# Kernel optimization log

Hardware: AMD Instinct MI355X
Metric: run time of the kernel (lower is better)

## Reference

```python
import jax, jax.numpy as jnp
import numpy as np

T, B, E, H = 2048, 2, 1024, 16
Dh = E // H


def setup_inputs() -> dict:
    key = jax.random.key(0)
    ks = jax.random.split(key, 5)
    s = 0.02
    query = jax.random.normal(ks[0], (T, B, E), dtype=jnp.float32)
    Wq = jax.random.normal(ks[1], (E, E), dtype=jnp.float32) * s
    Wk = jax.random.normal(ks[2], (E, E), dtype=jnp.float32) * s
    Wv = jax.random.normal(ks[3], (E, E), dtype=jnp.float32) * s
    Wo = jax.random.normal(ks[4], (E, E), dtype=jnp.float32) * s
    bq = jnp.zeros((E,), jnp.float32)
    bk = jnp.zeros((E,), jnp.float32)
    bv = jnp.zeros((E,), jnp.float32)
    bo = jnp.zeros((E,), jnp.float32)
    # additive causal mask: 0 on/below diagonal, -inf above (standard fairseq usage)
    neg = jnp.finfo(jnp.float32).min
    attn_mask = jnp.where(jnp.triu(jnp.ones((T, T), jnp.bool_), k=1), neg, 0.0).astype(jnp.float32)
    return {"query": query, "Wq": Wq, "bq": bq, "Wk": Wk, "bk": bk,
            "Wv": Wv, "bv": bv, "Wo": Wo, "bo": bo, "attn_mask": attn_mask}


def reference(query, Wq, bq, Wk, bk, Wv, bv, Wo, bo, attn_mask):
    t, b, e = query.shape
    scale = Dh ** -0.5
    # self-attention projections (nn.Linear: x @ W.T + b)
    q = (query @ Wq.T + bq) * scale  # [T,B,E]
    k = query @ Wk.T + bk
    v = query @ Wv.T + bv
    # [T, B*H, Dh] -> [B*H, T, Dh]
    q = q.reshape(t, b * H, Dh).transpose(1, 0, 2)
    k = k.reshape(t, b * H, Dh).transpose(1, 0, 2)
    v = v.reshape(t, b * H, Dh).transpose(1, 0, 2)
    # explicit bmm -> softmax -> bmm (materializes [B*H, T, T])
    attn_weights = jnp.einsum('btd,bsd->bts', q, k) + attn_mask[None, :, :]
    attn_probs = jax.nn.softmax(attn_weights, axis=-1)
    attn = jnp.einsum('bts,bsd->btd', attn_probs, v)  # [B*H, T, Dh]
    attn = attn.transpose(1, 0, 2).reshape(t, b, e)  # [T,B,E]
    out = attn @ Wo.T + bo
    return out
```

## Files before the change

### kernel.cpp

```cpp
#include <hip/hip_runtime.h>


typedef __attribute__((ext_vector_type(8))) short   s16x8;
typedef __attribute__((ext_vector_type(4))) float   f32x4;
typedef __attribute__((ext_vector_type(2))) __fp16  f16x2;
typedef __attribute__((ext_vector_type(4))) __fp16  f16x4;

#define MFMA16(a, b, c) __builtin_amdgcn_mfma_f32_16x16x32_bf16((a), (b), (c), 0, 0, 0)
#define MFMApv(a, b, c) __builtin_amdgcn_mfma_f32_16x16x16f16((a), (b), (c), 0, 0, 0)

static __device__ __forceinline__ unsigned short f2bf(float f) {
    unsigned u = __float_as_uint(f);
    unsigned r = u + 0x7fffu + ((u >> 16) & 1u);
    return (unsigned short)(r >> 16);
}

static __device__ __forceinline__ void gl2lds16(const void* g, void* l) {
    __builtin_amdgcn_global_load_lds(
        (const __attribute__((address_space(1))) unsigned int*)g,
        (__attribute__((address_space(3))) unsigned int*)l, 16, 0, 0);
}

__global__ __launch_bounds__(256) void cvt_all(const float* __restrict__ query,
                                               const float* __restrict__ w0,
                                               const float* __restrict__ w1,
                                               const float* __restrict__ w2,
                                               const float* __restrict__ w3,
                                               unsigned short* __restrict__ Xb,
                                               unsigned short* __restrict__ Wcat) {
    const int bx = blockIdx.x;
    if (bx < 4096) {
        const int i = threadIdx.x;
        const float4 f = reinterpret_cast<const float4*>(query + (size_t)bx * 1024)[i];
        ushort4 u;
        u.x = f2bf(f.x); u.y = f2bf(f.y); u.z = f2bf(f.z); u.w = f2bf(f.w);
        const int mrow = (bx & 1) * 2048 + (bx >> 1);
        reinterpret_cast<ushort4*>(Xb + (size_t)mrow * 1024)[i] = u;
    } else {
        const int j   = bx - 4096;
        const int sel = j >> 10;
        const int i   = (j & 1023) * 256 + threadIdx.x;
        const float* src = (sel == 0) ? w0 : (sel == 1) ? w1 : (sel == 2) ? w2 : w3;
        const float4 f = reinterpret_cast<const float4*>(src)[i];
        ushort4 u;
        u.x = f2bf(f.x); u.y = f2bf(f.y); u.z = f2bf(f.z); u.w = f2bf(f.w);
        reinterpret_cast<ushort4*>(Wcat + (size_t)sel * 1048576)[i] = u;
    }
}

__global__ __launch_bounds__(512, 2) void gemm_qkv(const unsigned short* __restrict__ A,
                                                   const unsigned short* __restrict__ W,
                                                   const float* __restrict__ b0,
                                                   const float* __restrict__ b1,
                                                   const float* __restrict__ b2,
                                                   unsigned short* __restrict__ outQK,
                                                   __fp16* __restrict__ outV) {
    __shared__ __align__(16) unsigned short smem[65536];

    const int tid  = threadIdx.x;
    const int w    = tid >> 6;
    const int lane = tid & 63;
    const int quad = lane >> 4;
    const int c    = lane & 15;
    const int wm   = w >> 2;
    const int wn   = w & 3;

    const int id   = blockIdx.x;
    const int xcd  = id & 7;
    const int slot = id >> 3;
    const int m0 = (xcd * 2 + (slot & 1)) * 256;
    const int n0 = (slot >> 1) * 256;

    f32x4 acc[8][4];
    #pragma unroll
    for (int mi = 0; mi < 8; ++mi)
        #pragma unroll
        for (int ni = 0; ni < 4; ++ni) acc[mi][ni] = (f32x4){0.f, 0.f, 0.f, 0.f};

    const int srow = tid >> 3;
    const int g    = (tid & 7) ^ (srow & 7);
    const unsigned short* aG = A + (size_t)(m0 + srow) * 1024 + g * 8;
    const unsigned short* wG = W + (size_t)(n0 + srow) * 1024 + g * 8;
    const int loff = tid * 8;

#define STA(buf, u, k0) gl2lds16(aG + (k0) + (u) * 65536, &smem[(buf) * 32768 + (u) * 4096 + loff])
#define STB(buf, u, k0) gl2lds16(wG + (k0) + (u) * 65536, &smem[(buf) * 32768 + 16384 + (u) * 4096 + loff])

    STB(0, 0, 0); STB(0, 1, 0); STB(0, 2, 0); STB(0, 3, 0);
    STA(0, 0, 0); STA(0, 2, 0); STA(0, 1, 0); STA(0, 3, 0);
    asm volatile("s_waitcnt vmcnt(2)" ::: "memory");
    asm volatile("s_barrier" ::: "memory");

    const int cs  = c & 7;
    const int ch0 = (quad ^ cs) << 3;
    const int ch1 = ((4 + quad) ^ cs) << 3;

    s16x8 af[4][2], bf[4][2];

    #pragma unroll
    for (int mi = 0; mi < 4; ++mi) {
        const int row = (wm * 128 + mi * 16 + c) * 64;
        af[mi][0] = *reinterpret_cast<const s16x8*>(&smem[row + ch0]);
        af[mi][1] = *reinterpret_cast<const s16x8*>(&smem[row + ch1]);
    }
    #pragma unroll
    for (int ni = 0; ni < 4; ++ni) {
        const int row = (wn * 64 + ni * 16 + c) * 64;
        bf[ni][0] = *reinterpret_cast<const s16x8*>(&smem[16384 + row + ch0]);
        bf[ni][1] = *reinterpret_cast<const s16x8*>(&smem[16384 + row + ch1]);
    }

    #pragma unroll 1
    for (int t = 0; t < 16; ++t) {
        const unsigned short* Al = &smem[(t & 1) * 32768];
        const int  nb   = (t & 1) ^ 1;
        const int  kn   = (t + 1) * 64;
        const bool more = (t < 15);

        if (more) {
            STB(nb, 0, kn); STB(nb, 1, kn); STB(nb, 2, kn); STB(nb, 3, kn);
            STA(nb, 0, kn); STA(nb, 2, kn); STA(nb, 1, kn); STA(nb, 3, kn);
        }

        __builtin_amdgcn_s_setprio(1);
        #pragma unroll
        for (int mi = 0; mi < 4; ++mi)
            #pragma unroll
            for (int ni = 0; ni < 4; ++ni) {
                acc[mi][ni] = MFMA16(af[mi][0], bf[ni][0], acc[mi][ni]);
                acc[mi][ni] = MFMA16(af[mi][1], bf[ni][1], acc[mi][ni]);
            }
        __builtin_amdgcn_s_setprio(0);

        if (more) asm volatile("s_waitcnt vmcnt(8)" ::: "memory");
        else      asm volatile("s_waitcnt vmcnt(0)" ::: "memory");
        asm volatile("s_barrier" ::: "memory");

        #pragma unroll
        for (int mi = 0; mi < 4; ++mi) {
            const int row = (wm * 128 + 64 + mi * 16 + c) * 64;
            af[mi][0] = *reinterpret_cast<const s16x8*>(&Al[row + ch0]);
            af[mi][1] = *reinterpret_cast<const s16x8*>(&Al[row + ch1]);
        }
        __builtin_amdgcn_s_setprio(1);
        #pragma unroll
        for (int mi = 0; mi < 4; ++mi)
            #pragma unroll
            for (int ni = 0; ni < 4; ++ni) {
                acc[4 + mi][ni] = MFMA16(af[mi][0], bf[ni][0], acc[4 + mi][ni]);
                acc[4 + mi][ni] = MFMA16(af[mi][1], bf[ni][1], acc[4 + mi][ni]);
            }
        __builtin_amdgcn_s_setprio(0);

        if (more) {
            asm volatile("s_waitcnt vmcnt(2)" ::: "memory");
            asm volatile("s_barrier" ::: "memory");
            const unsigned short* An = &smem[nb * 32768];
            #pragma unroll
            for (int mi = 0; mi < 4; ++mi) {
                const int row = (wm * 128 + mi * 16 + c) * 64;
                af[mi][0] = *reinterpret_cast<const s16x8*>(&An[row + ch0]);
                af[mi][1] = *reinterpret_cast<const s16x8*>(&An[row + ch1]);
            }
            #pragma unroll
            for (int ni = 0; ni < 4; ++ni) {
                const int row = (wn * 64 + ni * 16 + c) * 64;
                bf[ni][0] = *reinterpret_cast<const s16x8*>(&An[16384 + row + ch0]);
                bf[ni][1] = *reinterpret_cast<const s16x8*>(&An[16384 + row + ch1]);
            }
        }
    }
#undef STA
#undef STB

    if (n0 < 2048) {
        const float scale = (n0 < 1024) ? 0.18033688011112042f : 1.0f;
        const float* bias = (n0 < 1024) ? b0 : b1;
        #pragma unroll
        for (int ni = 0; ni < 4; ++ni) {
            const int n = n0 + wn * 64 + ni * 16 + c;
            const float bval = bias[n & 1023];
            #pragma unroll
            for (int mi = 0; mi < 8; ++mi)
                #pragma unroll
                for (int r = 0; r < 4; ++r) {
                    const int m = m0 + wm * 128 + mi * 16 + quad * 4 + r;
                    outQK[(size_t)m * 2048 + n] = f2bf((acc[mi][ni][r] + bval) * scale);
                }
        }
    } else {
        __fp16* lds16 = reinterpret_cast<__fp16*>(smem);
        #pragma unroll 1
        for (int tn = 0; tn < 2; ++tn) {
            __syncthreads();
            if ((wn >> 1) == tn) {
                #pragma unroll
                for (int ni = 0; ni < 4; ++ni) {
                    const int nLoc = (wn & 1) * 64 + ni * 16 + c;
                    const float bval = b2[(n0 - 2048) + tn * 128 + nLoc];
                    #pragma unroll
                    for (int mi = 0; mi < 8; ++mi) {
                        const int mLoc = mi * 16 + quad * 4;
                        const f16x2 lo = __builtin_amdgcn_cvt_pkrtz(acc[mi][ni][0] + bval,
                                                                    acc[mi][ni][1] + bval);
                        const f16x2 hi = __builtin_amdgcn_cvt_pkrtz(acc[mi][ni][2] + bval,
                                                                    acc[mi][ni][3] + bval);
                        uint2 st;
                        st.x = __builtin_bit_cast(unsigned int, lo);
                        st.y = __builtin_bit_cast(unsigned int, hi);
                        const int phys = wm * 16384 + nLoc * 128 +
                                         (((mLoc >> 3) ^ (nLoc & 15)) << 3) + (mLoc & 7);
                        *reinterpret_cast<uint2*>(&lds16[phys]) = st;
                    }
                }
            }
            __syncthreads();
            const int np   = tid >> 1;
            const int rg   = np >> 7;
            const int nLoc = np & 127;
            const int vcol = (n0 - 2048) + tn * 128 + nLoc;
            const int bb = m0 >> 11;
            const int tbase = (m0 & 2047) + rg * 128;
            __fp16* vdst = outV + ((size_t)((bb * 16 + (vcol >> 6)) * 64 + (vcol & 63))) * 2048 + tbase;
            #pragma unroll
            for (int j = 0; j < 8; ++j) {
                const int lc = (tid & 1) * 8 + j;
                *reinterpret_cast<uint4*>(vdst + lc * 8) =
                    *reinterpret_cast<const uint4*>(
                        &lds16[rg * 16384 + nLoc * 128 + ((lc ^ (nLoc & 15)) << 3)]);
            }
        }
    }
}

__global__ __launch_bounds__(256) void gemm_out(const unsigned short* __restrict__ A,
                                                const unsigned short* __restrict__ W,
                                                const float* __restrict__ bias,
                                                float* __restrict__ outF) {
    __shared__ __align__(16) unsigned short Al[2][64 * 64];
    __shared__ __align__(16) unsigned short Bl[2][128 * 64];

    const int tid  = threadIdx.x;
    const int w    = tid >> 6;
    const int lane = tid & 63;
    const int quad = lane >> 4;
    const int c    = lane & 15;

    const int id   = blockIdx.x;
    const int xcd  = id & 7;
    const int slot = id >> 3;
    const int m0 = (xcd * 8 + (slot & 7)) * 64;
    const int n0 = (slot >> 3) * 128;

    f32x4 acc[8];
    #pragma unroll
    for (int ni = 0; ni < 8; ++ni) acc[ni] = (f32x4){0.f, 0.f, 0.f, 0.f};

    const int srow = tid >> 3;
    const int g    = (tid & 7) ^ (srow & 7);
    const unsigned short* aG = A + (size_t)(m0 + srow) * 1024 + g * 8;
    const unsigned short* wG = W + (size_t)(n0 + srow) * 1024 + g * 8;
    const int loff = tid * 8;

    const int cs = (c & 7);

    gl2lds16(aG,             &Al[0][loff]);
    gl2lds16(aG + 32 * 1024, &Al[0][loff + 2048]);
    #pragma unroll
    for (int i = 0; i < 4; ++i)
        gl2lds16(wG + i * 32 * 1024, &Bl[0][loff + i * 2048]);

    #pragma unroll 1
    for (int kk = 0; kk < 16; ++kk) {
        __syncthreads();
        if (kk < 15) {
            const int k0n = (kk + 1) * 64;
            const int nb  = (kk + 1) & 1;
            gl2lds16(aG + k0n,             &Al[nb][loff]);
            gl2lds16(aG + k0n + 32 * 1024, &Al[nb][loff + 2048]);
            #pragma unroll
            for (int i = 0; i < 4; ++i)
                gl2lds16(wG + k0n + i * 32 * 1024, &Bl[nb][loff + i * 2048]);
        }
        const int cb = kk & 1;
        const int arow = (w * 16 + c) * 64;
        const s16x8 af0 = *reinterpret_cast<const s16x8*>(&Al[cb][arow + ((quad ^ cs) << 3)]);
        const s16x8 af1 = *reinterpret_cast<const s16x8*>(&Al[cb][arow + (((4 + quad) ^ cs) << 3)]);
        __builtin_amdgcn_s_setprio(1);
        #pragma unroll
        for (int ni = 0; ni < 8; ++ni) {
            const int brow = (ni * 16 + c) * 64;
            const s16x8 bf0 = *reinterpret_cast<const s16x8*>(&Bl[cb][brow + ((quad ^ cs) << 3)]);
            const s16x8 bf1 = *reinterpret_cast<const s16x8*>(&Bl[cb][brow + (((4 + quad) ^ cs) << 3)]);
            acc[ni] = MFMA16(af0, bf0, acc[ni]);
            acc[ni] = MFMA16(af1, bf1, acc[ni]);
        }
        __builtin_amdgcn_s_setprio(0);
    }

    #pragma unroll
    for (int ni = 0; ni < 8; ++ni) {
        const int n = n0 + ni * 16 + c;
        const float bval = bias[n];
        const int m = m0 + w * 16 + quad * 4;
        const int bb = m >> 11, t = m & 2047;
        #pragma unroll
        for (int r = 0; r < 4; ++r)
            outF[(size_t)(2 * (t + r) + bb) * 1024 + n] = acc[ni][r] + bval;
    }
}

__global__ __launch_bounds__(256, 4) void attn_kernel(const unsigned short* __restrict__ QKb,
                                                      const __fp16* __restrict__ Vt,
                                                      unsigned short* __restrict__ Ob) {
    __shared__ unsigned short Kl[2][2][64][32];
    __shared__ __fp16 Vl[2][64][64];

    const int tid  = threadIdx.x;
    const int w    = tid >> 6;
    const int lane = tid & 63;
    const int quad = lane >> 4;
    const int c    = lane & 15;

    const int id = blockIdx.x;
    const int bh = (id & 7) * 4 + ((id >> 3) & 3);
    const int kidx = id >> 5;
    const int rr   = kidx >> 3, jj = kidx & 7;
    const int a    = (rr & 1) ? (24 - 8 * rr + jj) : (31 - 8 * rr - jj);
    const int bB = bh >> 4, h = bh & 15;
    const int t0 = a * 64;
    const int trg = t0 + w * 16;
    const int nIt = a + 1;

    const unsigned short* qp = QKb + (size_t)(bB * 2048 + trg + c) * 2048 + h * 64 + quad * 8;
    const s16x8 aq0 = *reinterpret_cast<const s16x8*>(qp);
    const s16x8 aq1 = *reinterpret_cast<const s16x8*>(qp + 32);

    const int lr4 = lane >> 2, sl4 = lane & 3;
    const unsigned short* kSrc = QKb + (size_t)(bB * 2048 + w * 16 + lr4) * 2048
                                 + 1024 + h * 64 + (sl4 ^ ((lane >> 3) & 3)) * 8;
    const int vr8 = lane >> 3, sl8 = lane & 7;
    const __fp16* vSrcA = Vt + (size_t)(bh * 64 + w * 16 + vr8) * 2048 + (sl8 ^ vr8) * 8;
    const __fp16* vSrcB = vSrcA + (size_t)8 * 2048;

    f32x4 acc[4];
    float l = 0.f;
    #pragma unroll
    for (int dt = 0; dt < 4; ++dt) acc[dt] = (f32x4){0.f, 0.f, 0.f, 0.f};

    const int kswz = (quad ^ ((c >> 1) & 3)) * 8;

    {
        gl2lds16(kSrc,      &Kl[0][0][w * 16 + lr4][sl4 * 8]);
        gl2lds16(kSrc + 32, &Kl[0][1][w * 16 + lr4][sl4 * 8]);
        gl2lds16(vSrcA,     &Vl[0][w * 16 + vr8][sl8 * 8]);
        gl2lds16(vSrcB,     &Vl[0][w * 16 + 8 + vr8][sl8 * 8]);
    }

    for (int it = 0; it < nIt; ++it) {
        const int buf = it & 1;
        __syncthreads();
        if (it + 1 < nIt) {
            const size_t s1 = (size_t)(it + 1) * 64;
            const int nb = buf ^ 1;
            gl2lds16(kSrc + s1 * 2048,      &Kl[nb][0][w * 16 + lr4][sl4 * 8]);
            gl2lds16(kSrc + s1 * 2048 + 32, &Kl[nb][1][w * 16 + lr4][sl4 * 8]);
            gl2lds16(vSrcA + s1,            &Vl[nb][w * 16 + vr8][sl8 * 8]);
            gl2lds16(vSrcB + s1,            &Vl[nb][w * 16 + 8 + vr8][sl8 * 8]);
        }

        s16x8 kf[4][2];
        #pragma unroll
        for (int ns = 0; ns < 4; ++ns) {
            kf[ns][0] = *reinterpret_cast<const s16x8*>(&Kl[buf][0][ns * 16 + c][kswz]);
            kf[ns][1] = *reinterpret_cast<const s16x8*>(&Kl[buf][1][ns * 16 + c][kswz]);
        }
        f16x4 vf[4][4];
        #pragma unroll
        for (int dt = 0; dt < 4; ++dt)
            #pragma unroll
            for (int ch = 0; ch < 4; ++ch) {
                const int phys = ((2 * ch + (quad >> 1)) ^ (c & 7)) * 8 + (quad & 1) * 4;
                vf[dt][ch] = *reinterpret_cast<const f16x4*>(&Vl[buf][dt * 16 + c][phys]);
            }

        const int s0 = it * 64;
        const bool diag = (it == a);
        f32x4 sT[4];
        __builtin_amdgcn_s_setprio(1);
        #pragma unroll
        for (int ns = 0; ns < 4; ++ns) {
            f32x4 z = (f32x4){0.f, 0.f, 0.f, 0.f};
            z = MFMA16(kf[ns][0], aq0, z);
            sT[ns] = MFMA16(kf[ns][1], aq1, z);
        }
        __builtin_amdgcn_s_setprio(0);
        f16x4 pf[4];
        float lp = 0.f;
        #pragma unroll
        for (int ns = 0; ns < 4; ++ns) {
            float pv[4];
            #pragma unroll
            for (int r = 0; r < 4; ++r) pv[r] = __builtin_amdgcn_exp2f(sT[ns][r]);
            if (diag) {
                const int sb = s0 + ns * 16 + quad * 4;
                const int qg = trg + c;
                #pragma unroll
                for (int r = 0; r < 4; ++r) if (sb + r > qg) pv[r] = 0.f;
            }
            lp += (pv[0] + pv[1]) + (pv[2] + pv[3]);
            const f16x2 lo = __builtin_amdgcn_cvt_pkrtz(pv[0], pv[1]);
            const f16x2 hi = __builtin_amdgcn_cvt_pkrtz(pv[2], pv[3]);
            pf[ns] = __builtin_shufflevector(lo, hi, 0, 1, 2, 3);
        }
        l += lp;
        __builtin_amdgcn_s_setprio(1);
        #pragma unroll
        for (int dt = 0; dt < 4; ++dt)
            #pragma unroll
            for (int ns = 0; ns < 4; ++ns)
                acc[dt] = MFMApv(vf[dt][ns], pf[ns], acc[dt]);
        __builtin_amdgcn_s_setprio(0);
    }

    float lv = l;
    lv += __shfl_xor(lv, 16);
    lv += __shfl_xor(lv, 32);
    const float inv = 1.0f / lv;
    const size_t base = (size_t)(bB * 2048 + trg + c) * 1024 + h * 64;
    #pragma unroll
    for (int dt = 0; dt < 4; ++dt) {
        const unsigned u0 = (unsigned)f2bf(acc[dt][0] * inv)
                          | ((unsigned)f2bf(acc[dt][1] * inv) << 16);
        const unsigned u1 = (unsigned)f2bf(acc[dt][2] * inv)
                          | ((unsigned)f2bf(acc[dt][3] * inv) << 16);
        uint2 st; st.x = u0; st.y = u1;
        *reinterpret_cast<uint2*>(Ob + base + dt * 16 + quad * 4) = st;
    }
}

extern "C" void kernel_launch(void* const* d_in, const int* in_sizes, int n_in,
                              void* d_out, int out_size, void* d_ws, size_t ws_size,
                              hipStream_t stream) {
    const float* query = (const float*)d_in[0];
    const float* Wq    = (const float*)d_in[1];
    const float* bq    = (const float*)d_in[2];
    const float* Wk    = (const float*)d_in[3];
    const float* bk    = (const float*)d_in[4];
    const float* Wv    = (const float*)d_in[5];
    const float* bv    = (const float*)d_in[6];
    const float* Wo    = (const float*)d_in[7];
    const float* bo    = (const float*)d_in[8];

    float* out = (float*)d_out;

    unsigned short* ws    = (unsigned short*)d_ws;
    unsigned short* Xbf   = ws;
    unsigned short* Wcat  = Xbf  + (size_t)4096 * 1024;
    unsigned short* QKb   = Wcat + (size_t)4 * 1024 * 1024;
    __fp16*         Vtw   = (__fp16*)(QKb + (size_t)4096 * 2048);
    unsigned short* attnb = (unsigned short*)(Vtw + (size_t)32 * 64 * 2048);

    cvt_all<<<8192, 256, 0, stream>>>(query, Wq, Wk, Wv, Wo, Xbf, Wcat);

    gemm_qkv<<<192, 512, 0, stream>>>(Xbf, Wcat, bq, bk, bv, QKb, Vtw);

    attn_kernel<<<1024, 256, 0, stream>>>(QKb, Vtw, attnb);

    gemm_out<<<512, 256, 0, stream>>>(attnb, Wcat + (size_t)3 * 1024 * 1024,
                                      bo, out);
}
```

Baseline: 193.5 us.

## Shrink QKV GEMM N-tile to 192 so grid fills all 256 CUs

The QKV projection GEMM's output tile width drops from 256 to 192 columns. The grid grows from 192 to 256 blocks, matching the CU count on MI355X and removing idle CUs. The epilogue is reworked so a tile can straddle the K/V boundary (column 2048): QK columns take the bf16 path, V columns go through a reworked LDS transpose into the fp16 transposed V buffer. The smaller tile lowers arithmetic intensity per block and adds branchy epilogue logic.

```diff
diff --git a/kernel.cpp b/kernel.cpp
--- a/kernel.cpp
+++ b/kernel.cpp
@@ -55,7 +55,7 @@
                                                    const float* __restrict__ b2,
                                                    unsigned short* __restrict__ outQK,
                                                    __fp16* __restrict__ outV) {
-    __shared__ __align__(16) unsigned short smem[65536];
+    __shared__ __align__(16) unsigned short smem[57344];
 
     const int tid  = threadIdx.x;
     const int w    = tid >> 6;
@@ -69,13 +69,13 @@
     const int xcd  = id & 7;
     const int slot = id >> 3;
     const int m0 = (xcd * 2 + (slot & 1)) * 256;
-    const int n0 = (slot >> 1) * 256;
-
-    f32x4 acc[8][4];
+    const int n0 = (slot >> 1) * 192;
+
+    f32x4 acc[8][3];
     #pragma unroll
     for (int mi = 0; mi < 8; ++mi)
         #pragma unroll
-        for (int ni = 0; ni < 4; ++ni) acc[mi][ni] = (f32x4){0.f, 0.f, 0.f, 0.f};
+        for (int ni = 0; ni < 3; ++ni) acc[mi][ni] = (f32x4){0.f, 0.f, 0.f, 0.f};
 
     const int srow = tid >> 3;
     const int g    = (tid & 7) ^ (srow & 7);
@@ -83,10 +83,10 @@
     const unsigned short* wG = W + (size_t)(n0 + srow) * 1024 + g * 8;
     const int loff = tid * 8;
 
-#define STA(buf, u, k0) gl2lds16(aG + (k0) + (u) * 65536, &smem[(buf) * 32768 + (u) * 4096 + loff])
-#define STB(buf, u, k0) gl2lds16(wG + (k0) + (u) * 65536, &smem[(buf) * 32768 + 16384 + (u) * 4096 + loff])
-
-    STB(0, 0, 0); STB(0, 1, 0); STB(0, 2, 0); STB(0, 3, 0);
+#define STA(buf, u, k0) gl2lds16(aG + (k0) + (u) * 65536, &smem[(buf) * 28672 + (u) * 4096 + loff])
+#define STB(buf, u, k0) gl2lds16(wG + (k0) + (u) * 65536, &smem[(buf) * 28672 + 16384 + (u) * 4096 + loff])
+
+    STB(0, 0, 0); STB(0, 1, 0); STB(0, 2, 0);
     STA(0, 0, 0); STA(0, 2, 0); STA(0, 1, 0); STA(0, 3, 0);
     asm volatile("s_waitcnt vmcnt(2)" ::: "memory");
     asm volatile("s_barrier" ::: "memory");
@@ -95,7 +95,7 @@
     const int ch0 = (quad ^ cs) << 3;
     const int ch1 = ((4 + quad) ^ cs) << 3;
 
-    s16x8 af[4][2], bf[4][2];
+    s16x8 af[4][2], bf[3][2];
 
     #pragma unroll
     for (int mi = 0; mi < 4; ++mi) {
@@ -104,21 +104,21 @@
         af[mi][1] = *reinterpret_cast<const s16x8*>(&smem[row + ch1]);
     }
     #pragma unroll
-    for (int ni = 0; ni < 4; ++ni) {
-        const int row = (wn * 64 + ni * 16 + c) * 64;
+    for (int ni = 0; ni < 3; ++ni) {
+        const int row = (wn * 48 + ni * 16 + c) * 64;
         bf[ni][0] = *reinterpret_cast<const s16x8*>(&smem[16384 + row + ch0]);
         bf[ni][1] = *reinterpret_cast<const s16x8*>(&smem[16384 + row + ch1]);
     }
 
     #pragma unroll 1
     for (int t = 0; t < 16; ++t) {
-        const unsigned short* Al = &smem[(t & 1) * 32768];
+        const unsigned short* Al = &smem[(t & 1) * 28672];
         const int  nb   = (t & 1) ^ 1;
         const int  kn   = (t + 1) * 64;
         const bool more = (t < 15);
 
         if (more) {
-            STB(nb, 0, kn); STB(nb, 1, kn); STB(nb, 2, kn); STB(nb, 3, kn);
+            STB(nb, 0, kn); STB(nb, 1, kn); STB(nb, 2, kn);
             STA(nb, 0, kn); STA(nb, 2, kn); STA(nb, 1, kn); STA(nb, 3, kn);
         }
 
@@ -126,13 +126,13 @@
         #pragma unroll
         for (int mi = 0; mi < 4; ++mi)
             #pragma unroll
-            for (int ni = 0; ni < 4; ++ni) {
+            for (int ni = 0; ni < 3; ++ni) {
                 acc[mi][ni] = MFMA16(af[mi][0], bf[ni][0], acc[mi][ni]);
                 acc[mi][ni] = MFMA16(af[mi][1], bf[ni][1], acc[mi][ni]);
             }
         __builtin_amdgcn_s_setprio(0);
 
-        if (more) asm volatile("s_waitcnt vmcnt(8)" ::: "memory");
+        if (more) asm volatile("s_waitcnt vmcnt(7)" ::: "memory");
         else      asm volatile("s_waitcnt vmcnt(0)" ::: "memory");
         asm volatile("s_barrier" ::: "memory");
 
@@ -146,7 +146,7 @@
         #pragma unroll
         for (int mi = 0; mi < 4; ++mi)
             #pragma unroll
-            for (int ni = 0; ni < 4; ++ni) {
+            for (int ni = 0; ni < 3; ++ni) {
                 acc[4 + mi][ni] = MFMA16(af[mi][0], bf[ni][0], acc[4 + mi][ni]);
                 acc[4 + mi][ni] = MFMA16(af[mi][1], bf[ni][1], acc[4 + mi][ni]);
             }
@@ -155,7 +155,7 @@
         if (more) {
             asm volatile("s_waitcnt vmcnt(2)" ::: "memory");
             asm volatile("s_barrier" ::: "memory");
-            const unsigned short* An = &smem[nb * 32768];
+            const unsigned short* An = &smem[nb * 28672];
             #pragma unroll
             for (int mi = 0; mi < 4; ++mi) {
                 const int row = (wm * 128 + mi * 16 + c) * 64;
@@ -163,8 +163,8 @@
                 af[mi][1] = *reinterpret_cast<const s16x8*>(&An[row + ch1]);
             }
             #pragma unroll
-            for (int ni = 0; ni < 4; ++ni) {
-                const int row = (wn * 64 + ni * 16 + c) * 64;
+            for (int ni = 0; ni < 3; ++ni) {
+                const int row = (wn * 48 + ni * 16 + c) * 64;
                 bf[ni][0] = *reinterpret_cast<const s16x8*>(&An[16384 + row + ch0]);
                 bf[ni][1] = *reinterpret_cast<const s16x8*>(&An[16384 + row + ch1]);
             }
@@ -173,13 +173,13 @@
 #undef STA
 #undef STB
 
-    if (n0 < 2048) {
-        const float scale = (n0 < 1024) ? 0.18033688011112042f : 1.0f;
-        const float* bias = (n0 < 1024) ? b0 : b1;
-        #pragma unroll
-        for (int ni = 0; ni < 4; ++ni) {
-            const int n = n0 + wn * 64 + ni * 16 + c;
-            const float bval = bias[n & 1023];
+    const float qs = 0.18033688011112042f;
+    #pragma unroll
+    for (int ni = 0; ni < 3; ++ni) {
+        const int n = n0 + wn * 48 + ni * 16 + c;
+        if (n < 2048) {
+            const float bval  = (n < 1024) ? b0[n] : b1[n & 1023];
+            const float scale = (n < 1024) ? qs : 1.0f;
             #pragma unroll
             for (int mi = 0; mi < 8; ++mi)
                 #pragma unroll
@@ -188,46 +188,45 @@
                     outQK[(size_t)m * 2048 + n] = f2bf((acc[mi][ni][r] + bval) * scale);
                 }
         }
-    } else {
+    }
+
+    if (n0 >= 1920) {
+        const int vg0 = (n0 >= 2048) ? (n0 - 2048) : 0;
+        const int nV  = n0 + 192 - ((n0 > 2048) ? n0 : 2048);
         __fp16* lds16 = reinterpret_cast<__fp16*>(smem);
-        #pragma unroll 1
-        for (int tn = 0; tn < 2; ++tn) {
-            __syncthreads();
-            if ((wn >> 1) == tn) {
+        __syncthreads();
+        #pragma unroll
+        for (int ni = 0; ni < 3; ++ni) {
+            const int n = n0 + wn * 48 + ni * 16 + c;
+            if (n >= 2048) {
+                const int lv = (n - 2048) - vg0;
+                const float bval = b2[n - 2048];
                 #pragma unroll
-                for (int ni = 0; ni < 4; ++ni) {
-                    const int nLoc = (wn & 1) * 64 + ni * 16 + c;
-                    const float bval = b2[(n0 - 2048) + tn * 128 + nLoc];
-                    #pragma unroll
-                    for (int mi = 0; mi < 8; ++mi) {
-                        const int mLoc = mi * 16 + quad * 4;
-                        const f16x2 lo = __builtin_amdgcn_cvt_pkrtz(acc[mi][ni][0] + bval,
-                                                                    acc[mi][ni][1] + bval);
-                        const f16x2 hi = __builtin_amdgcn_cvt_pkrtz(acc[mi][ni][2] + bval,
-                                                                    acc[mi][ni][3] + bval);
-                        uint2 st;
-                        st.x = __builtin_bit_cast(unsigned int, lo);
-                        st.y = __builtin_bit_cast(unsigned int, hi);
-                        const int phys = wm * 16384 + nLoc * 128 +
-                                         (((mLoc >> 3) ^ (nLoc & 15)) << 3) + (mLoc & 7);
-                        *reinterpret_cast<uint2*>(&lds16[phys]) = st;
-                    }
+                for (int mi = 0; mi < 8; ++mi) {
+                    const int m = wm * 128 + mi * 16 + quad * 4;
+                    const f16x2 lo = __builtin_amdgcn_cvt_pkrtz(acc[mi][ni][0] + bval,
+                                                                acc[mi][ni][1] + bval);
+                    const f16x2 hi = __builtin_amdgcn_cvt_pkrtz(acc[mi][ni][2] + bval,
+                                                                acc[mi][ni][3] + bval);
+                    uint2 st;
+                    st.x = __builtin_bit_cast(unsigned int, lo);
+                    st.y = __builtin_bit_cast(unsigned int, hi);
+                    const int phys = lv * 256 + (((m >> 3) ^ (lv & 31)) << 3) + (m & 7);
+                    *reinterpret_cast<uint2*>(&lds16[phys]) = st;
                 }
             }
-            __syncthreads();
-            const int np   = tid >> 1;
-            const int rg   = np >> 7;
-            const int nLoc = np & 127;
-            const int vcol = (n0 - 2048) + tn * 128 + nLoc;
-            const int bb = m0 >> 11;
-            const int tbase = (m0 & 2047) + rg * 128;
+        }
+        __syncthreads();
+        const int lv = tid >> 1;
+        if (lv < nV) {
+            const int vcol = vg0 + lv;
+            const int bb = m0 >> 11, tbase = m0 & 2047;
             __fp16* vdst = outV + ((size_t)((bb * 16 + (vcol >> 6)) * 64 + (vcol & 63))) * 2048 + tbase;
             #pragma unroll
-            for (int j = 0; j < 8; ++j) {
-                const int lc = (tid & 1) * 8 + j;
+            for (int j = 0; j < 16; ++j) {
+                const int lc = (tid & 1) * 16 + j;
                 *reinterpret_cast<uint4*>(vdst + lc * 8) =
-                    *reinterpret_cast<const uint4*>(
-                        &lds16[rg * 16384 + nLoc * 128 + ((lc ^ (nLoc & 15)) << 3)]);
+                    *reinterpret_cast<const uint4*>(&lds16[lv * 256 + ((lc ^ (lv & 31)) << 3)]);
             }
         }
     }
@@ -463,7 +462,7 @@
 
     cvt_all<<<8192, 256, 0, stream>>>(query, Wq, Wk, Wv, Wo, Xbf, Wcat);
 
-    gemm_qkv<<<192, 512, 0, stream>>>(Xbf, Wcat, bq, bk, bv, QKb, Vtw);
+    gemm_qkv<<<256, 512, 0, stream>>>(Xbf, Wcat, bq, bk, bv, QKb, Vtw);
 
     attn_kernel<<<1024, 256, 0, stream>>>(QKb, Vtw, attnb);
 
```

New measurement: 187.3 us. -3.2%, faster.
